# Kernel tuning notes

Hardware: AMD Instinct MI355X
Metric: run time of the kernel (lower is better)

Reference implementation:

```python
import jax, jax.numpy as jnp
import numpy as np

B, N, DIM = 1, 2048, 2048
H, KVH = 32, 4                 # query heads, kv heads
D = DIM // H                   # head_dim = 64
REP = H // KVH                 # queries per kv = 8
KV_DIM = D * KVH               # 256


def _rope_tables(n, d, base=10000.0):
    inv = 1.0 / (base ** (np.arange(0, d, 2, dtype=np.float32) / d))
    t = np.arange(n, dtype=np.float32)
    freqs = np.outer(t, inv)                      # [n, d/2]
    emb = np.concatenate([freqs, freqs], axis=-1)  # [n, d]
    return jnp.asarray(np.cos(emb)), jnp.asarray(np.sin(emb))


def setup_inputs() -> dict:
    key = jax.random.key(0)
    ks = jax.random.split(key, 5)
    s = 0.02
    cos, sin = _rope_tables(N, D)
    return {
        "x": jax.random.normal(ks[0], (B, N, DIM), jnp.float32),
        "Wq": jax.random.normal(ks[1], (DIM, DIM), jnp.float32) * s,
        "Wk": jax.random.normal(ks[2], (KV_DIM, DIM), jnp.float32) * s,
        "Wv": jax.random.normal(ks[3], (KV_DIM, DIM), jnp.float32) * s,
        "Wo": jax.random.normal(ks[4], (DIM, DIM), jnp.float32) * s,
        "cos": cos,
        "sin": sin,
    }


def _rotate_half(t):
    d2 = t.shape[-1] // 2
    return jnp.concatenate([-t[..., d2:], t[..., :d2]], axis=-1)


def reference(x, Wq, Wk, Wv, Wo, cos, sin):
    b, n, _ = x.shape
    # projections (nn.Linear: x @ W.T)
    q = (x @ Wq.T).reshape(b, n, H, D).transpose(0, 2, 1, 3)     # b h n d
    k = (x @ Wk.T).reshape(b, n, KVH, D).transpose(0, 2, 1, 3)   # b g n d
    v = (x @ Wv.T).reshape(b, n, KVH, D).transpose(0, 2, 1, 3)
    # RoPE
    c = cos[None, None, :, :]
    s = sin[None, None, :, :]
    q = q * c + _rotate_half(q) * s
    k = k * c + _rotate_half(k) * s
    # expand KV heads (repeat_interleave over head dim)
    k = jnp.repeat(k, REP, axis=1)   # b h n d
    v = jnp.repeat(v, REP, axis=1)
    # causal attention with materialized scores (faithful to source)
    scale = 1.0 / jnp.sqrt(jnp.asarray(D, x.dtype))
    scores = jnp.einsum('bhld,bhsd->bhls', q, k) * scale
    causal = jnp.tril(jnp.ones((n, n), bool))
    scores = jnp.where(causal[None, None], scores, jnp.asarray(-jnp.inf, x.dtype))
    attn = jax.nn.softmax(scores, axis=-1)
    y = jnp.einsum('bhls,bhsd->bhld', attn, v)       # b h n d
    y = y.transpose(0, 2, 1, 3).reshape(b, n, DIM)   # b n (h d)
    return y @ Wo.T
```

## Files before the change

kernel.cpp:

```cpp
#include <hip/hip_runtime.h>

typedef unsigned short u16;
typedef __attribute__((ext_vector_type(8))) short short8;
typedef __attribute__((ext_vector_type(4))) float floatx4;

#define N_TOK 2048
#define DIM   2048
#define NH    32
#define NKVH  4
#define HD    64
#define KVD   256

__device__ __forceinline__ float bf2f(u16 u) {
  union { unsigned i; float f; } c; c.i = ((unsigned)u) << 16; return c.f;
}
__device__ __forceinline__ u16 f2bf(float f) {
  union { float f; unsigned i; } c; c.f = f;
  unsigned x = c.i;
  return (u16)((x + 0x7fffu + ((x >> 16) & 1u)) >> 16);
}

__device__ __forceinline__ void gload16(const u16* g, u16* l) {
#if defined(__has_builtin) && __has_builtin(__builtin_amdgcn_global_load_lds)
  __builtin_amdgcn_global_load_lds(
      (const __attribute__((address_space(1))) void*)g,
      (__attribute__((address_space(3))) void*)l, 16, 0, 0);
#else
  *(short8*)l = *(const short8*)g;
#endif
}

#define C_X  1048576
#define C_WQ 2097152
#define C_WK 2228224
#define C_WV 2359296
#define C_WO 3407872
__global__ __launch_bounds__(256) void cvt_all(const float* __restrict__ x,
                                               const float* __restrict__ wq,
                                               const float* __restrict__ wk,
                                               const float* __restrict__ wv,
                                               const float* __restrict__ wo,
                                               u16* __restrict__ dst) {
  int i = blockIdx.x * 256 + threadIdx.x;
  const float* src; int off;
  if      (i < C_X)  { src = x;  off = 0; }
  else if (i < C_WQ) { src = wq; off = C_X; }
  else if (i < C_WK) { src = wk; off = C_WQ; }
  else if (i < C_WV) { src = wv; off = C_WK; }
  else               { src = wo; off = C_WV; }
  float4 v = ((const float4*)src)[i - off];
  ushort4 o;
  o.x = f2bf(v.x); o.y = f2bf(v.y); o.z = f2bf(v.z); o.w = f2bf(v.w);
  ((ushort4*)dst)[i] = o;
}


__global__ __launch_bounds__(256) void gemm_qkv(const u16* __restrict__ A,
                                                const u16* __restrict__ Wq,
                                                const u16* __restrict__ Wk,
                                                const u16* __restrict__ Wv,
                                                const float* __restrict__ cs,
                                                const float* __restrict__ sn,
                                                u16* __restrict__ Qp,
                                                u16* __restrict__ Kp,
                                                u16* __restrict__ Vp) {
  __shared__ __align__(16) u16 As[64 * 32];
  __shared__ __align__(16) u16 Bs[128 * 32];
  const int tid  = threadIdx.x;
  const int lane = tid & 63;
  const int w    = tid >> 6;
  const int r    = lane & 15, q = lane >> 4;
  const int tm = blockIdx.x & 31;
  const int tn = blockIdx.x >> 5;
  const int wm = w & 1, wn = w >> 1;
  const int K = DIM;

  const u16* W; int wrow0;
  if (tn < 16)      { W = Wq; wrow0 = tn * 128; }
  else if (tn < 18) { W = Wk; wrow0 = (tn - 16) * 128; }
  else              { W = Wv; wrow0 = (tn - 18) * 128; }

  const int srow = tid >> 2;
  const int scol = (tid & 3) * 8;
  const u16* ga = A + (size_t)(tm * 64 + srow) * K + scol;
  const u16* gb = W + (size_t)(wrow0 + srow) * K + scol;
  u16* lA = &As[tid * 8];
  u16* lB = &Bs[tid * 8];

  floatx4 acc[2][4];
#pragma unroll
  for (int a = 0; a < 2; ++a)
#pragma unroll
    for (int b = 0; b < 4; ++b) acc[a][b] = (floatx4){0.f, 0.f, 0.f, 0.f};

  for (int k0 = 0; k0 < K; k0 += 32) {
    __syncthreads();
    gload16(ga + k0, lA);
    gload16(gb + k0, lB);
    gload16(gb + k0 + (size_t)64 * K, lB + 2048);
    __syncthreads();

    short8 af[2], bf[4];
#pragma unroll
    for (int mi = 0; mi < 2; ++mi)
      af[mi] = *(const short8*)&As[(wm * 32 + mi * 16 + r) * 32 + q * 8];
#pragma unroll
    for (int nj = 0; nj < 4; ++nj)
      bf[nj] = *(const short8*)&Bs[(wn * 64 + nj * 16 + r) * 32 + q * 8];
#pragma unroll
    for (int mi = 0; mi < 2; ++mi)
#pragma unroll
      for (int nj = 0; nj < 4; ++nj)
        acc[mi][nj] = __builtin_amdgcn_mfma_f32_16x16x32_bf16(af[mi], bf[nj], acc[mi][nj], 0, 0, 0);
  }

  if (tn < 18) {
    const int head = (tn < 16) ? (tn * 2 + wn) : ((tn - 16) * 2 + wn);
#pragma unroll
    for (int mi = 0; mi < 2; ++mi)
#pragma unroll
      for (int g = 0; g < 4; ++g) {
        int row = tm * 64 + wm * 32 + mi * 16 + 4 * q + g;
        const float* crow  = cs + (size_t)row * 64;
        const float* srow2 = sn + (size_t)row * 64;
#pragma unroll
        for (int nj = 0; nj < 2; ++nj) {
          int d = nj * 16 + r;
          float x0 = acc[mi][nj][g];
          float x1 = acc[mi][nj + 2][g];
          float o0 = x0 * crow[d]      - x1 * srow2[d];
          float o1 = x1 * crow[d + 32] + x0 * srow2[d + 32];
          int qq = d >> 3, j = d & 7;
          int lslot = (qq * 16 + (row & 15)) * 8 + j;
          if (tn < 16) {
            int sq = row >> 5, ii = (row >> 4) & 1;
            size_t base = ((size_t)(head * 64 + sq) * 4 + ii * 2) * 512 + lslot;
            Qp[base]       = f2bf(o0);
            Qp[base + 512] = f2bf(o1);
          } else {
            int kt = row >> 6, t = (row >> 4) & 3;
            size_t base = ((size_t)(head * 32 + kt) * 8 + t * 2) * 512 + lslot;
            Kp[base]       = f2bf(o0);
            Kp[base + 512] = f2bf(o1);
          }
        }
      }
  } else {
#pragma unroll
    for (int mi = 0; mi < 2; ++mi)
#pragma unroll
      for (int nj = 0; nj < 4; ++nj) {
        int col  = (tn - 18) * 128 + wn * 64 + nj * 16 + r;
        int kvh  = col >> 6;
        int t    = (col & 63) >> 4;
        int rr   = col & 15;
        int row0 = tm * 64 + wm * 32 + mi * 16 + 4 * q;
        int kt   = row0 >> 6;
        int wk   = row0 & 63;
        int s    = wk >> 5;
        int qq   = (wk & 31) >> 3;
        int j0   = wk & 7;
        uint2 pk;
        pk.x = (unsigned)f2bf(acc[mi][nj][0]) | ((unsigned)f2bf(acc[mi][nj][1]) << 16);
        pk.y = (unsigned)f2bf(acc[mi][nj][2]) | ((unsigned)f2bf(acc[mi][nj][3]) << 16);
        size_t idx = ((size_t)(kvh * 32 + kt) * 8 + s * 4 + t) * 512 + (qq * 16 + rr) * 8 + j0;
        *(uint2*)(Vp + idx) = pk;
      }
  }
}

__global__ __launch_bounds__(256) void gemm_out(const u16* __restrict__ A,
                                                const u16* __restrict__ W,
                                                float* __restrict__ C) {
  __shared__ __align__(16) u16 As[64 * 32];
  __shared__ __align__(16) u16 Bs[128 * 32];
  const int tid  = threadIdx.x;
  const int lane = tid & 63;
  const int w    = tid >> 6;
  const int r    = lane & 15, q = lane >> 4;
  const int tn = blockIdx.x & 15;
  const int tm = blockIdx.x >> 4;
  const int wm = w & 1, wn = w >> 1;
  const int K = DIM;

  const int srow = tid >> 2;
  const int scol = (tid & 3) * 8;
  const u16* ga = A + (size_t)(tm * 64 + srow) * K + scol;
  const u16* gb = W + (size_t)(tn * 128 + srow) * K + scol;
  u16* lA = &As[tid * 8];
  u16* lB = &Bs[tid * 8];

  floatx4 acc[2][4];
#pragma unroll
  for (int a = 0; a < 2; ++a)
#pragma unroll
    for (int b = 0; b < 4; ++b) acc[a][b] = (floatx4){0.f, 0.f, 0.f, 0.f};

  for (int k0 = 0; k0 < K; k0 += 32) {
    __syncthreads();
    gload16(ga + k0, lA);
    gload16(gb + k0, lB);
    gload16(gb + k0 + (size_t)64 * K, lB + 2048);
    __syncthreads();

    short8 af[2], bf[4];
#pragma unroll
    for (int mi = 0; mi < 2; ++mi)
      af[mi] = *(const short8*)&As[(wm * 32 + mi * 16 + r) * 32 + q * 8];
#pragma unroll
    for (int nj = 0; nj < 4; ++nj)
      bf[nj] = *(const short8*)&Bs[(wn * 64 + nj * 16 + r) * 32 + q * 8];
#pragma unroll
    for (int mi = 0; mi < 2; ++mi)
#pragma unroll
      for (int nj = 0; nj < 4; ++nj)
        acc[mi][nj] = __builtin_amdgcn_mfma_f32_16x16x32_bf16(af[mi], bf[nj], acc[mi][nj], 0, 0, 0);
  }

#pragma unroll
  for (int mi = 0; mi < 2; ++mi)
#pragma unroll
    for (int g = 0; g < 4; ++g) {
      int row = tm * 64 + wm * 32 + mi * 16 + 4 * q + g;
#pragma unroll
      for (int nj = 0; nj < 4; ++nj)
        C[(size_t)row * DIM + tn * 128 + wn * 64 + nj * 16 + r] = acc[mi][nj][g];
    }
}

__global__ __launch_bounds__(64, 2) void attn_mfma(const u16* __restrict__ Qp,
                                                   const u16* __restrict__ Kp,
                                                   const u16* __restrict__ Vp,
                                                   u16* __restrict__ Yb) {
  __shared__ __align__(16) u16 Pl[32][72];
  const int lane = threadIdx.x;
  const int r    = lane & 15;
  const int q    = lane >> 4;
  const int bx   = blockIdx.x;
  const int qt   = 15 - (bx >> 2);
  const int sub  = 3 - (bx & 3);
  const int h    = blockIdx.y;
  const int kvh  = h >> 3;
  const int baseq = qt * 128 + sub * 32;
  const int sq   = baseq >> 5;
  const int ktmax = (baseq + 31) >> 6;

  short8 qf[2][2];
#pragma unroll
  for (int i = 0; i < 2; ++i)
#pragma unroll
    for (int c = 0; c < 2; ++c)
      qf[i][c] = *(const short8*)(Qp + ((size_t)(h * 64 + sq) * 4 + i * 2 + c) * 512 + lane * 8);

  floatx4 O[2][4];
  float lsum[2];
#pragma unroll
  for (int i = 0; i < 2; ++i) {
    lsum[i] = 0.f;
#pragma unroll
    for (int t = 0; t < 4; ++t) O[i][t] = (floatx4){0.f, 0.f, 0.f, 0.f};
  }

  const u16* Kbase = Kp + (size_t)(kvh * 32) * 8 * 512;
  const u16* Vbase = Vp + (size_t)(kvh * 32) * 8 * 512;

  auto loadK = [&](int kt, short8 (&kf)[4][2]) {
    const u16* kb = Kbase + (size_t)kt * 8 * 512 + lane * 8;
#pragma unroll
    for (int t = 0; t < 4; ++t) {
      kf[t][0] = *(const short8*)(kb + (t * 2 + 0) * 512);
      kf[t][1] = *(const short8*)(kb + (t * 2 + 1) * 512);
    }
  };

  auto body = [&](int kt, short8 (&kc)[4][2], short8 (&kn)[4][2]) {
    short8 vb[2][4];
    {
      const u16* vbp = Vbase + (size_t)kt * 8 * 512 + lane * 8;
#pragma unroll
      for (int s = 0; s < 2; ++s)
#pragma unroll
        for (int t = 0; t < 4; ++t)
          vb[s][t] = *(const short8*)(vbp + (s * 4 + t) * 512);
    }

    loadK(kt < ktmax ? kt + 1 : ktmax, kn);

    floatx4 ST[2][4];
#pragma unroll
    for (int i = 0; i < 2; ++i)
#pragma unroll
      for (int t = 0; t < 4; ++t) ST[i][t] = (floatx4){0.f, 0.f, 0.f, 0.f};
#pragma unroll
    for (int t = 0; t < 4; ++t)
#pragma unroll
      for (int i = 0; i < 2; ++i) {
        ST[i][t] = __builtin_amdgcn_mfma_f32_16x16x32_bf16(kc[t][0], qf[i][0], ST[i][t], 0, 0, 0);
        ST[i][t] = __builtin_amdgcn_mfma_f32_16x16x32_bf16(kc[t][1], qf[i][1], ST[i][t], 0, 0, 0);
      }

    if (kt == ktmax) {
#pragma unroll
      for (int i = 0; i < 2; ++i) {
        int qrow = baseq + 16 * i + r;
#pragma unroll
        for (int t = 0; t < 4; ++t) {
          int key = kt * 64 + 16 * t + 4 * q;
#pragma unroll
          for (int g = 0; g < 4; ++g)
            if (key + g > qrow) ST[i][t][g] = -1e30f;
        }
      }
    }

#pragma unroll
    for (int i = 0; i < 2; ++i)
#pragma unroll
      for (int t = 0; t < 4; ++t) {
        float p0 = __expf(0.125f * ST[i][t][0]);
        float p1 = __expf(0.125f * ST[i][t][1]);
        float p2 = __expf(0.125f * ST[i][t][2]);
        float p3 = __expf(0.125f * ST[i][t][3]);
        lsum[i] += (p0 + p1) + (p2 + p3);
        uint2 pk;
        pk.x = (unsigned)f2bf(p0) | ((unsigned)f2bf(p1) << 16);
        pk.y = (unsigned)f2bf(p2) | ((unsigned)f2bf(p3) << 16);
        *(uint2*)&Pl[16 * i + r][16 * t + 4 * q] = pk;
      }

#pragma unroll
    for (int s = 0; s < 2; ++s)
#pragma unroll
      for (int i = 0; i < 2; ++i) {
        short8 pa = *(const short8*)&Pl[16 * i + r][32 * s + 8 * q];
#pragma unroll
        for (int t = 0; t < 4; ++t)
          O[i][t] = __builtin_amdgcn_mfma_f32_16x16x32_bf16(pa, vb[s][t], O[i][t], 0, 0, 0);
      }
  };

  short8 kA[4][2], kB[4][2];
  loadK(0, kA);
  for (int kt = 0; kt <= ktmax; kt += 2) {
    body(kt, kA, kB);
    if (kt + 1 <= ktmax) body(kt + 1, kB, kA);
  }

#pragma unroll
  for (int i = 0; i < 2; ++i) {
    lsum[i] += __shfl_xor(lsum[i], 16);
    lsum[i] += __shfl_xor(lsum[i], 32);
  }

#pragma unroll
  for (int i = 0; i < 2; ++i) {
    float inv[4];
#pragma unroll
    for (int g = 0; g < 4; ++g)
      inv[g] = 1.f / __shfl(lsum[i], 4 * q + g);
#pragma unroll
    for (int g = 0; g < 4; ++g) {
      u16* yp = Yb + (size_t)(baseq + 16 * i + 4 * q + g) * DIM + h * 64 + r;
      yp[0]  = f2bf(O[i][0][g] * inv[g]);
      yp[16] = f2bf(O[i][1][g] * inv[g]);
      yp[32] = f2bf(O[i][2][g] * inv[g]);
      yp[48] = f2bf(O[i][3][g] * inv[g]);
    }
  }
}

extern "C" void kernel_launch(void* const* d_in, const int* in_sizes, int n_in,
                              void* d_out, int out_size, void* d_ws, size_t ws_size,
                              hipStream_t stream) {
  const float* x  = (const float*)d_in[0];
  const float* Wq = (const float*)d_in[1];
  const float* Wk = (const float*)d_in[2];
  const float* Wv = (const float*)d_in[3];
  const float* Wo = (const float*)d_in[4];
  const float* cs = (const float*)d_in[5];
  const float* sn = (const float*)d_in[6];

  u16* ws  = (u16*)d_ws;
  u16* xb  = ws;
  u16* Wqb = xb  + (size_t)N_TOK * DIM;
  u16* Wkb = Wqb + (size_t)DIM * DIM;
  u16* Wvb = Wkb + (size_t)KVD * DIM;
  u16* Wob = Wvb + (size_t)KVD * DIM;
  u16* Qp  = Wob + (size_t)DIM * DIM;
  u16* Kp  = Qp  + (size_t)N_TOK * DIM;
  u16* Vp  = Kp  + (size_t)N_TOK * KVD;
  u16* Yb  = Vp  + (size_t)N_TOK * KVD;

  cvt_all<<<dim3(13312), 256, 0, stream>>>(x, Wq, Wk, Wv, Wo, ws);

  gemm_qkv<<<dim3(640), 256, 0, stream>>>(xb, Wqb, Wkb, Wvb, cs, sn, Qp, Kp, Vp);

  attn_mfma<<<dim3(64, 32), 64, 0, stream>>>(Qp, Kp, Vp, Yb);

  gemm_out<<<dim3(512), 256, 0, stream>>>(Yb, Wob, (float*)d_out);
}
```

Measured before the change: 225.9 us.

## Split attention key loop across two waves per block and combine partials

The attention kernel now launches two wavefronts per block. Each wave processes alternate 64-key tiles (even or odd), keeping its own P staging buffer in shared memory. At the end, the second wave writes its partial O accumulators and row sums to LDS, and the first wave adds them in and normalises. This doubles the parallelism per query tile to cut the latency of long causal rows, at the cost of an LDS reduction, a block barrier, and more shared memory per block.

```diff
diff --git a/kernel.cpp b/kernel.cpp
--- a/kernel.cpp
+++ b/kernel.cpp
@@ -228,12 +228,16 @@
     }
 }
 
-__global__ __launch_bounds__(64, 2) void attn_mfma(const u16* __restrict__ Qp,
-                                                   const u16* __restrict__ Kp,
-                                                   const u16* __restrict__ Vp,
-                                                   u16* __restrict__ Yb) {
-  __shared__ __align__(16) u16 Pl[32][72];
-  const int lane = threadIdx.x;
+__global__ __launch_bounds__(128, 2) void attn_mfma(const u16* __restrict__ Qp,
+                                                    const u16* __restrict__ Kp,
+                                                    const u16* __restrict__ Vp,
+                                                    u16* __restrict__ Yb) {
+  __shared__ __align__(16) u16 Pl[2][32][72];
+  __shared__ float Ocmb[32][66];
+  __shared__ float Lcmb[2][64];
+  const int tid  = threadIdx.x;
+  const int lane = tid & 63;
+  const int w    = tid >> 6;
   const int r    = lane & 15;
   const int q    = lane >> 4;
   const int bx   = blockIdx.x;
@@ -284,7 +288,7 @@
           vb[s][t] = *(const short8*)(vbp + (s * 4 + t) * 512);
     }
 
-    loadK(kt < ktmax ? kt + 1 : ktmax, kn);
+    loadK(kt + 2 <= ktmax ? kt + 2 : ktmax, kn);
 
     floatx4 ST[2][4];
 #pragma unroll
@@ -325,14 +329,14 @@
         uint2 pk;
         pk.x = (unsigned)f2bf(p0) | ((unsigned)f2bf(p1) << 16);
         pk.y = (unsigned)f2bf(p2) | ((unsigned)f2bf(p3) << 16);
-        *(uint2*)&Pl[16 * i + r][16 * t + 4 * q] = pk;
+        *(uint2*)&Pl[w][16 * i + r][16 * t + 4 * q] = pk;
       }
 
 #pragma unroll
     for (int s = 0; s < 2; ++s)
 #pragma unroll
       for (int i = 0; i < 2; ++i) {
-        short8 pa = *(const short8*)&Pl[16 * i + r][32 * s + 8 * q];
+        short8 pa = *(const short8*)&Pl[w][16 * i + r][32 * s + 8 * q];
 #pragma unroll
         for (int t = 0; t < 4; ++t)
           O[i][t] = __builtin_amdgcn_mfma_f32_16x16x32_bf16(pa, vb[s][t], O[i][t], 0, 0, 0);
@@ -340,10 +344,36 @@
   };
 
   short8 kA[4][2], kB[4][2];
-  loadK(0, kA);
-  for (int kt = 0; kt <= ktmax; kt += 2) {
-    body(kt, kA, kB);
-    if (kt + 1 <= ktmax) body(kt + 1, kB, kA);
+  const int kt0 = w;
+  if (kt0 <= ktmax) {
+    loadK(kt0, kA);
+    for (int kt = kt0; kt <= ktmax; kt += 4) {
+      body(kt, kA, kB);
+      if (kt + 2 <= ktmax) body(kt + 2, kB, kA);
+    }
+  }
+
+  if (w == 1) {
+#pragma unroll
+    for (int i = 0; i < 2; ++i) {
+#pragma unroll
+      for (int t = 0; t < 4; ++t)
+#pragma unroll
+        for (int g = 0; g < 4; ++g)
+          Ocmb[(i * 4 + t) * 4 + g][lane] = O[i][t][g];
+      Lcmb[i][lane] = lsum[i];
+    }
+  }
+  __syncthreads();
+  if (w == 1) return;
+#pragma unroll
+  for (int i = 0; i < 2; ++i) {
+#pragma unroll
+    for (int t = 0; t < 4; ++t)
+#pragma unroll
+      for (int g = 0; g < 4; ++g)
+        O[i][t][g] += Ocmb[(i * 4 + t) * 4 + g][lane];
+    lsum[i] += Lcmb[i][lane];
   }
 
 #pragma unroll
@@ -395,7 +425,7 @@
 
   gemm_qkv<<<dim3(640), 256, 0, stream>>>(xb, Wqb, Wkb, Wvb, cs, sn, Qp, Kp, Vp);
 
-  attn_mfma<<<dim3(64, 32), 64, 0, stream>>>(Qp, Kp, Vp, Yb);
+  attn_mfma<<<dim3(64, 32), 128, 0, stream>>>(Qp, Kp, Vp, Yb);
 
   gemm_out<<<dim3(512), 256, 0, stream>>>(Yb, Wob, (float*)d_out);
 }
```

After: 224.0 us. About the same (-0.8%).
